# Kernel tuning notes

Measured on AMD Instinct MI355X. Metric: run time of the kernel, lower is better.

## Reference

```python
import jax, jax.numpy as jnp
import numpy as np

B, S, D, H, HD = 4, 2048, 1024, 16, 64


def setup_inputs() -> dict:
    key = jax.random.key(0)
    k1, k2, k3 = jax.random.split(key, 3)
    x = jax.random.normal(k1, (B, S, D), dtype=jnp.float32)
    w_attn = jax.random.normal(k2, (D, 3, H, HD), dtype=jnp.float32) * 0.02
    b_attn = jnp.zeros((3, H, HD), dtype=jnp.float32)
    w_proj = jax.random.normal(k3, (H, HD, D), dtype=jnp.float32) * 0.02
    b_proj = jnp.zeros((D,), dtype=jnp.float32)
    return {"x": x, "w_attn": w_attn, "b_attn": b_attn, "w_proj": w_proj, "b_proj": b_proj}


def reference(x, w_attn, b_attn, w_proj, b_proj):
    # c_attn: [B,S,D] x [D,3,H,HD] -> [B,3,H,S,HD]
    qkv = jnp.einsum('bsd,dqhe->bqhse', x, w_attn) + b_attn[None, :, :, None, :]
    q, k, v = qkv[:, 0], qkv[:, 1], qkv[:, 2]  # each [B,H,S,HD]
    scale = 1.0 / jnp.sqrt(jnp.asarray(HD, dtype=q.dtype))
    scores = jnp.einsum('bhse,bhte->bhst', q * scale, k)  # [B,H,S,S]
    causal = jnp.tril(jnp.ones((S, S), dtype=bool))
    scores = jnp.where(causal, scores, jnp.asarray(-1e9, dtype=scores.dtype))
    attn = jax.nn.softmax(scores, axis=-1)
    out = jnp.einsum('bhst,bhte->bhse', attn, v)  # [B,H,S,HD]
    # c_proj: contract (heads, head_size) -> embed
    return jnp.einsum('bhse,hed->bsd', out, w_proj) + b_proj
```

## Files before the change

kernel.cpp:

```cpp
#include <hip/hip_runtime.h>

#define NB 4
#define NS 2048
#define ND 1024
#define NH 16
#define NE 64
#define NM (NB*NS)

typedef __attribute__((ext_vector_type(8))) __bf16 bf16x8;
typedef __attribute__((ext_vector_type(4))) float f32x4;

__device__ __forceinline__ float bf2f(unsigned short h) {
  union { unsigned u; float f; } c; c.u = ((unsigned)h) << 16; return c.f;
}
__device__ __forceinline__ unsigned short f2bf(float f) {
  union { float f; unsigned u; } c; c.f = f;
  return (unsigned short)((c.u + 0x7fffu + ((c.u >> 16) & 1u)) >> 16);
}
__device__ __forceinline__ void load16_to_lds(const void* g, void* l) {
  __builtin_amdgcn_global_load_lds(
      (__attribute__((address_space(1))) void*)(void*)(unsigned long long)(const char*)g,
      (__attribute__((address_space(3))) void*)l, 16, 0, 0);
}

__global__ void detect_dtype(const unsigned* __restrict__ x, int* __restrict__ flag) {
  __shared__ int cnt;
  if (threadIdx.x == 0) cnt = 0;
  __syncthreads();
  unsigned w = x[((unsigned)threadIdx.x * 16381u) & ((1u << 21) - 1u)];
  unsigned lo = w & 0xFFFFu;
  int e = (int)((lo >> 7) & 0xFF);
  int plausible = (lo == 0u) || (e >= 100 && e <= 142);
  atomicAdd(&cnt, plausible);
  __syncthreads();
  if (threadIdx.x == 0) *flag = (cnt >= 192) ? 1 : 0;
}

__global__ void conv_to_bf16(const void* __restrict__ src, unsigned short* __restrict__ dst,
                             int n, const int* __restrict__ flag) {
  int stride = gridDim.x * blockDim.x;
  int i0 = blockIdx.x * blockDim.x + threadIdx.x;
  if (*flag) {
    const unsigned short* s = (const unsigned short*)src;
    for (int i = i0; i < n; i += stride) dst[i] = s[i];
  } else {
    const float* s = (const float*)src;
    for (int i = i0; i < n; i += stride) dst[i] = f2bf(s[i]);
  }
}

__global__ __launch_bounds__(256) void transpose_conv(const void* __restrict__ in,
                                                      unsigned short* __restrict__ out,
                                                      int K, int N, const int* __restrict__ flag) {
  __shared__ unsigned short tile[32][33];
  int n0 = blockIdx.x * 32, k0 = blockIdx.y * 32;
  int tx = threadIdx.x, ty = threadIdx.y;
  if (*flag) {
    const unsigned short* p = (const unsigned short*)in;
#pragma unroll
    for (int i = 0; i < 4; ++i)
      tile[ty + 8*i][tx] = p[(size_t)(k0 + ty + 8*i) * N + n0 + tx];
  } else {
    const float* p = (const float*)in;
#pragma unroll
    for (int i = 0; i < 4; ++i)
      tile[ty + 8*i][tx] = f2bf(p[(size_t)(k0 + ty + 8*i) * N + n0 + tx]);
  }
  __syncthreads();
#pragma unroll
  for (int i = 0; i < 4; ++i)
    out[(size_t)(n0 + ty + 8*i) * K + k0 + tx] = tile[tx][ty + 8*i];
}

#define BUFB 49152

__device__ __forceinline__ void gemm_core_v5(const unsigned short* __restrict__ Ag,
                                             const unsigned short* __restrict__ Btg,
                                             int m0, int n0,
                                             unsigned short* sm,
                                             f32x4 (&acc)[4][4]) {
  char* smb = (char*)sm;
  const int t = threadIdx.x;
  const int lane = t & 63, w = t >> 6;
  const int wr = w >> 1, wc = w & 1;
  const int frm = lane & 15, qd = lane >> 4;
  const int px0 = ((qd    ) ^ (frm & 7)) * 16;
  const int px1 = ((4 + qd) ^ (frm & 7)) * 16;
  const int NT = ND / 64;

  auto stage = [&](int kt, int b) {
    char* Ab = smb + b * BUFB;
    char* Bb = Ab + 32768;
    int kk = kt * 64;
#pragma unroll
    for (int u = 0; u < 4; ++u) {
      int ci = u * 512 + t;
      int row = ci >> 3, c = ci & 7, l = c ^ (row & 7);
      load16_to_lds(Ag + (size_t)(m0 + row) * ND + kk + l * 8, Ab + ci * 16);
    }
#pragma unroll
    for (int u = 0; u < 2; ++u) {
      int ci = u * 512 + t;
      int row = ci >> 3, c = ci & 7, l = c ^ (row & 7);
      load16_to_lds(Btg + (size_t)(n0 + row) * ND + kk + l * 8, Bb + ci * 16);
    }
  };

  stage(0, 0);
  asm volatile("s_waitcnt vmcnt(0)\n\ts_barrier" ::: "memory");

  for (int kt = 0; kt < NT; ++kt) {
    const int cur = kt & 1;
    const char* Ab = smb + cur * BUFB;
    const char* Bb = Ab + 32768;

    if (kt + 1 < NT) stage(kt + 1, cur ^ 1);

    bf16x8 a[4][2], b[4][2];
#pragma unroll
    for (int i = 0; i < 4; ++i) {
      int row = 64*wr + 16*i + frm;
      a[i][0] = *(const bf16x8*)(Ab + row * 128 + px0);
      a[i][1] = *(const bf16x8*)(Ab + row * 128 + px1);
    }
#pragma unroll
    for (int j = 0; j < 4; ++j) {
      int row = 64*wc + 16*j + frm;
      b[j][0] = *(const bf16x8*)(Bb + row * 128 + px0);
      b[j][1] = *(const bf16x8*)(Bb + row * 128 + px1);
    }
    asm volatile("s_waitcnt lgkmcnt(0)" ::: "memory");
    __builtin_amdgcn_s_setprio(1);
#pragma unroll
    for (int i = 0; i < 4; ++i)
#pragma unroll
      for (int j = 0; j < 4; ++j) {
        acc[i][j] = __builtin_amdgcn_mfma_f32_16x16x32_bf16(a[i][0], b[j][0], acc[i][j], 0, 0, 0);
        acc[i][j] = __builtin_amdgcn_mfma_f32_16x16x32_bf16(a[i][1], b[j][1], acc[i][j], 0, 0, 0);
      }
    __builtin_amdgcn_s_setprio(0);
    if (kt + 1 < NT)
      asm volatile("s_waitcnt vmcnt(0)\n\ts_barrier" ::: "memory");
  }
}

__global__ __launch_bounds__(512, 2) void gemm_qkv_v5(const unsigned short* __restrict__ X,
                                                      const unsigned short* __restrict__ W1T,
                                                      const unsigned short* __restrict__ battn,
                                                      unsigned short* __restrict__ qb,
                                                      unsigned short* __restrict__ kb,
                                                      unsigned short* __restrict__ vb) {
  __shared__ unsigned short sm[2 * 384 * 64];
  int flat = blockIdx.x + 24 * blockIdx.y;
  int virt = (flat & 7) * 96 + (flat >> 3);
  const int n0 = (virt % 24) * 128;
  const int m0 = (virt / 24) * 256;

  f32x4 acc[4][4] = {};
  gemm_core_v5(X, W1T, m0, n0, sm, acc);

  const int t = threadIdx.x, lane = t & 63, w = t >> 6;
  const int wr = w >> 1, wc = w & 1;
  const int coln = lane & 15, rbase = (lane >> 4) * 4;
#pragma unroll
  for (int j = 0; j < 4; ++j) {
    int nn = n0 + 64*wc + 16*j + coln;
    int qq = nn >> 10;
    int h  = (nn >> 6) & 15;
    int e  = nn & 63;
    float bias = bf2f(battn[nn]);
    float scale = (qq == 0) ? (0.125f * 1.44269504f) : 1.0f;
    if (qq == 2) {
#pragma unroll
      for (int i = 0; i < 4; ++i) {
        int mm0 = m0 + 64*wr + 16*i + rbase;
        int bb = mm0 >> 11, s0 = mm0 & 2047;
        unsigned long long pk = 0;
#pragma unroll
        for (int rr = 0; rr < 4; ++rr) {
          float v = acc[i][j][rr] + bias;
          pk |= ((unsigned long long)f2bf(v)) << (16 * rr);
        }
        size_t idx = (((size_t)bb * NH + h) * NE + e) * NS + s0;
        *(unsigned long long*)(vb + idx) = pk;
      }
    } else {
      unsigned short* dst = (qq == 0) ? qb : kb;
#pragma unroll
      for (int i = 0; i < 4; ++i) {
#pragma unroll
        for (int rr = 0; rr < 4; ++rr) {
          int mm = m0 + 64*wr + 16*i + rbase + rr;
          int bb = mm >> 11, s = mm & 2047;
          float v = (acc[i][j][rr] + bias) * scale;
          dst[(((size_t)bb * NH + h) * NS + s) * NE + e] = f2bf(v);
        }
      }
    }
  }
}

__global__ __launch_bounds__(512, 2) void gemm_proj_v5(const unsigned short* __restrict__ A,
                                                       const unsigned short* __restrict__ W2T,
                                                       const unsigned short* __restrict__ bproj,
                                                       void* __restrict__ outv,
                                                       const int* __restrict__ flag) {
  __shared__ unsigned short sm[2 * 384 * 64];
  int flat = blockIdx.x + 8 * blockIdx.y;
  int virt = (flat & 7) * 32 + (flat >> 3);
  const int n0 = (virt % 8) * 128;
  const int m0 = (virt / 8) * 256;

  f32x4 acc[4][4] = {};
  gemm_core_v5(A, W2T, m0, n0, sm, acc);

  const int isbf = *flag;
  unsigned short* out16 = (unsigned short*)outv;
  float* out32 = (float*)outv;
  const int t = threadIdx.x, lane = t & 63, w = t >> 6;
  const int wr = w >> 1, wc = w & 1;
  const int coln = lane & 15, rbase = (lane >> 4) * 4;
#pragma unroll
  for (int j = 0; j < 4; ++j) {
    int nn = n0 + 64*wc + 16*j + coln;
    float bias = bf2f(bproj[nn]);
#pragma unroll
    for (int i = 0; i < 4; ++i) {
#pragma unroll
      for (int rr = 0; rr < 4; ++rr) {
        int mm = m0 + 64*wr + 16*i + rbase + rr;
        float v = acc[i][j][rr] + bias;
        if (isbf) out16[(size_t)mm * ND + nn] = f2bf(v);
        else      out32[(size_t)mm * ND + nn] = v;
      }
    }
  }
}

__global__ __launch_bounds__(256, 4) void attn_causal(const unsigned short* __restrict__ qb,
                                                      const unsigned short* __restrict__ kb,
                                                      const unsigned short* __restrict__ vtb,
                                                      unsigned short* __restrict__ ob) {
  __shared__ unsigned short QPs[128 * 64];
  __shared__ unsigned short Ks[2][32 * 64];
  __shared__ unsigned short Vt[2][32 * 64];

  int t = threadIdx.x, lane = t & 63, w = t >> 6;
  int qd = lane >> 4, li = lane & 15;
  int sw0 = ((qd ^ (li & 7)) * 8);
  int sw1 = (((4 + qd) ^ (li & 7)) * 8);

  const int qtab[4][4] = {{15,8,7,0},{14,9,6,1},{13,10,5,2},{12,11,4,3}};
  int bi = blockIdx.x;
  int bh = bi & 63;
  int qt = qtab[(bi >> 6) & 3][bi >> 8];
  int q0 = qt * 128;
  int NT = 4 * qt + 4;
  size_t base = (size_t)bh * NS * NE;
  int bb = bh >> 4, hh = bh & 15;

  bf16x8 onesf;
#pragma unroll
  for (int j = 0; j < 8; ++j) onesf[j] = (__bf16)1.0f;

  auto stage_kv = [&](int kt, int buf) {
    int k0 = kt * 32;
    int r = t >> 3, p = t & 7, l = p ^ (r & 7);
    load16_to_lds(kb + base + (size_t)(k0 + r) * NE + l * 8, (char*)Ks[buf] + t * 16);
    int e = 2 * r + (l >> 2);
    load16_to_lds(vtb + base + (size_t)e * NS + k0 + (l & 3) * 8, (char*)Vt[buf] + t * 16);
  };

#pragma unroll
  for (int c = 0; c < 4; ++c) {
    int ch = c * 256 + t;
    int r = ch >> 3, jl = (ch & 7) ^ (r & 7);
    load16_to_lds(qb + base + (size_t)(q0 + r) * NE + jl * 8, (char*)QPs + ch * 16);
  }
  stage_kv(0, 0);
  asm volatile("s_waitcnt vmcnt(2)\n\ts_barrier" ::: "memory");

  bf16x8 qa[2][2];
#pragma unroll
  for (int i = 0; i < 2; ++i) {
    const unsigned short* qr = QPs + (32*w + 16*i + li) * 64;
    qa[i][0] = *(const bf16x8*)(qr + sw0);
    qa[i][1] = *(const bf16x8*)(qr + sw1);
  }

  f32x4 o[2][4] = {};
  float l_run[2][4] = {};

  for (int kt = 0; kt < NT; ++kt) {
    int cur = kt & 1;
    asm volatile("s_waitcnt lgkmcnt(0)\n\ts_barrier" ::: "memory");
    if (kt + 1 < NT) {
      stage_kv(kt + 1, cur ^ 1);
      asm volatile("s_waitcnt vmcnt(2)\n\ts_barrier" ::: "memory");
    } else {
      asm volatile("s_waitcnt vmcnt(0)\n\ts_barrier" ::: "memory");
    }

    int k0 = kt * 32;
    const unsigned short* Ksc = Ks[cur];
    const unsigned short* Vtc = Vt[cur];

    bf16x8 kfr[2][2];
#pragma unroll
    for (int c = 0; c < 2; ++c) {
      const unsigned short* kr = Ksc + (16*c + li) * 64;
      kfr[c][0] = *(const bf16x8*)(kr + sw0);
      kfr[c][1] = *(const bf16x8*)(kr + sw1);
    }

    int need_mask = (k0 >= q0);
#pragma unroll
    for (int i = 0; i < 2; ++i) {
#pragma unroll
      for (int c = 0; c < 2; ++c) {
        f32x4 s = {};
        s = __builtin_amdgcn_mfma_f32_16x16x32_bf16(qa[i][0], kfr[c][0], s, 0, 0, 0);
        s = __builtin_amdgcn_mfma_f32_16x16x32_bf16(qa[i][1], kfr[c][1], s, 0, 0, 0);
#pragma unroll
        for (int rr = 0; rr < 4; ++rr) {
          float pv = exp2f(s[rr]);
          if (need_mask) {
            int colk = k0 + 16*c + li;
            int rowq = q0 + 32*w + 16*i + qd*4 + rr;
            if (colk > rowq) pv = 0.f;
          }
          int prow = 32*w + 16*i + qd*4 + rr;
          int lo = 2*c + (li >> 3);
          QPs[prow * 64 + ((lo ^ (prow & 7)) * 8) + (li & 7)] =
              (unsigned short)(__float_as_uint(pv) >> 16);
        }
      }
    }

    bf16x8 pa[2];
#pragma unroll
    for (int i = 0; i < 2; ++i)
      pa[i] = *(const bf16x8*)(QPs + (32*w + 16*i + li) * 64 + sw0);

#pragma unroll
    for (int i = 0; i < 2; ++i) {
      f32x4 sm = {};
      sm = __builtin_amdgcn_mfma_f32_16x16x32_bf16(pa[i], onesf, sm, 0, 0, 0);
#pragma unroll
      for (int rr = 0; rr < 4; ++rr) l_run[i][rr] += sm[rr];
    }

#pragma unroll
    for (int c2 = 0; c2 < 4; ++c2) {
      const unsigned short* vr = Vtc + (8*c2 + (li >> 1)) * 64;
      bf16x8 vf = *(const bf16x8*)(vr + ((((li & 1) * 4 + qd) ^ ((li >> 1) & 7)) * 8));
#pragma unroll
      for (int i = 0; i < 2; ++i)
        o[i][c2] = __builtin_amdgcn_mfma_f32_16x16x32_bf16(pa[i], vf, o[i][c2], 0, 0, 0);
    }
  }

#pragma unroll
  for (int i = 0; i < 2; ++i)
#pragma unroll
    for (int c = 0; c < 4; ++c)
#pragma unroll
      for (int rr = 0; rr < 4; ++rr) {
        int rowm = 32*w + 16*i + qd*4 + rr;
        float inv = 1.0f / fmaxf(l_run[i][rr], 1e-30f);
        float ov = o[i][c][rr] * inv;
        int e = 16*c + li;
        ob[(((size_t)bb * NS + (q0 + rowm)) * NH + hh) * NE + e] = f2bf(ov);
      }
}

extern "C" void kernel_launch(void* const* d_in, const int* in_sizes, int n_in,
                              void* d_out, int out_size, void* d_ws, size_t ws_size,
                              hipStream_t stream) {
  (void)in_sizes; (void)n_in; (void)out_size; (void)ws_size;
  char* ws = (char*)d_ws;
  unsigned short* W1T = (unsigned short*)(ws);
  unsigned short* W2T = (unsigned short*)(ws + 6291456);
  unsigned short* qb  = (unsigned short*)(ws + 8388608);
  unsigned short* kb  = (unsigned short*)(ws + 25165824);
  unsigned short* vb  = (unsigned short*)(ws + 41943040);
  unsigned short* ob  = (unsigned short*)(ws + 58720256);
  unsigned short* bac = (unsigned short*)(ws + 75497472);
  unsigned short* bpc = (unsigned short*)(ws + 75505664);
  int*            flg = (int*)(ws + 75513856);
  unsigned short* xc  = ob;

  detect_dtype<<<1, 256, 0, stream>>>((const unsigned*)d_in[0], flg);
  conv_to_bf16<<<2048, 256, 0, stream>>>(d_in[0], xc,  NB*NS*ND, flg);
  conv_to_bf16<<<12,   256, 0, stream>>>(d_in[2], bac, 3*NH*NE, flg);
  conv_to_bf16<<<4,    256, 0, stream>>>(d_in[4], bpc, ND, flg);

  transpose_conv<<<dim3(3072/32, 1024/32), dim3(32, 8), 0, stream>>>(d_in[1], W1T, 1024, 3072, flg);
  transpose_conv<<<dim3(1024/32, 1024/32), dim3(32, 8), 0, stream>>>(d_in[3], W2T, 1024, 1024, flg);
  gemm_qkv_v5<<<dim3(3072/128, NM/256), 512, 0, stream>>>(xc, W1T, bac, qb, kb, vb);
  attn_causal<<<dim3(1024), 256, 0, stream>>>(qb, kb, vb, ob);
  gemm_proj_v5<<<dim3(1024/128, NM/256), 512, 0, stream>>>(ob, W2T, bpc, d_out, flg);
}
```

Baseline: 263.4 us.

## Enlarge attention tiles to 256 queries by 64 keys with 512-thread blocks

The causal attention kernel now has each block handle 256 query rows with 8 waves, and each step processes 64 keys instead of 32. Half as many blocks are launched, and the causal work-balancing table pairs short and long query chunks. Staging pointers are precomputed and advanced each step, the row-sum accumulation goes straight into an MFMA accumulator, and s_setprio raises wave priority around the MFMA sections. The aim is more K/V reuse per staged load and fewer barriers per key, at the cost of more LDS per block, fewer resident blocks, and coarser causal load balance.

```diff
diff --git a/kernel.cpp b/kernel.cpp
--- a/kernel.cpp
+++ b/kernel.cpp
@@ -237,25 +237,25 @@
   }
 }
 
-__global__ __launch_bounds__(256, 4) void attn_causal(const unsigned short* __restrict__ qb,
+__global__ __launch_bounds__(512, 4) void attn_causal(const unsigned short* __restrict__ qb,
                                                       const unsigned short* __restrict__ kb,
                                                       const unsigned short* __restrict__ vtb,
                                                       unsigned short* __restrict__ ob) {
-  __shared__ unsigned short QPs[128 * 64];
-  __shared__ unsigned short Ks[2][32 * 64];
-  __shared__ unsigned short Vt[2][32 * 64];
+  __shared__ unsigned short QPs[256 * 64];
+  __shared__ unsigned short Ks[2][64 * 64];
+  __shared__ unsigned short Vt[2][2 * 32 * 64];
 
   int t = threadIdx.x, lane = t & 63, w = t >> 6;
   int qd = lane >> 4, li = lane & 15;
   int sw0 = ((qd ^ (li & 7)) * 8);
   int sw1 = (((4 + qd) ^ (li & 7)) * 8);
 
-  const int qtab[4][4] = {{15,8,7,0},{14,9,6,1},{13,10,5,2},{12,11,4,3}};
+  const int tab[4][2] = {{0,7},{1,6},{2,5},{3,4}};
   int bi = blockIdx.x;
   int bh = bi & 63;
-  int qt = qtab[(bi >> 6) & 3][bi >> 8];
-  int q0 = qt * 128;
-  int NT = 4 * qt + 4;
+  int qc = tab[(bi >> 6) & 3][bi >> 8];
+  int q0 = qc * 256;
+  int NT = 4 * qc + 4;
   size_t base = (size_t)bh * NS * NE;
   int bb = bh >> 4, hh = bh & 15;
 
@@ -263,21 +263,31 @@
 #pragma unroll
   for (int j = 0; j < 8; ++j) onesf[j] = (__bf16)1.0f;
 
-  auto stage_kv = [&](int kt, int buf) {
-    int k0 = kt * 32;
-    int r = t >> 3, p = t & 7, l = p ^ (r & 7);
-    load16_to_lds(kb + base + (size_t)(k0 + r) * NE + l * 8, (char*)Ks[buf] + t * 16);
-    int e = 2 * r + (l >> 2);
-    load16_to_lds(vtb + base + (size_t)e * NS + k0 + (l & 3) * 8, (char*)Vt[buf] + t * 16);
+  int r8 = t >> 3;
+  int lswk = (t & 7) ^ (r8 & 7);
+  const char* ksrc = (const char*)(kb + base + (size_t)r8 * NE + lswk * 8);
+  char* kdst = (char*)Ks[0] + t * 16;
+  int sub = t >> 8, tt = t & 255;
+  int rv = tt >> 3;
+  int lswv = (tt & 7) ^ (rv & 7);
+  int ev = 2 * rv + (lswv >> 2);
+  const char* vsrc = (const char*)(vtb + base + (size_t)ev * NS + sub * 32 + (lswv & 3) * 8);
+  char* vdst = (char*)Vt[0] + sub * 4096 + tt * 16;
+
+  auto stage_kv = [&](int buf) {
+    load16_to_lds(ksrc, kdst + buf * 8192);
+    load16_to_lds(vsrc, vdst + buf * 8192);
+    ksrc += (size_t)64 * NE * 2;
+    vsrc += 64 * 2;
   };
 
 #pragma unroll
   for (int c = 0; c < 4; ++c) {
-    int ch = c * 256 + t;
+    int ch = c * 512 + t;
     int r = ch >> 3, jl = (ch & 7) ^ (r & 7);
     load16_to_lds(qb + base + (size_t)(q0 + r) * NE + jl * 8, (char*)QPs + ch * 16);
   }
-  stage_kv(0, 0);
+  stage_kv(0);
   asm volatile("s_waitcnt vmcnt(2)\n\ts_barrier" ::: "memory");
 
   bf16x8 qa[2][2];
@@ -289,35 +299,36 @@
   }
 
   f32x4 o[2][4] = {};
-  float l_run[2][4] = {};
+  f32x4 lacc[2] = {};
 
   for (int kt = 0; kt < NT; ++kt) {
     int cur = kt & 1;
     asm volatile("s_waitcnt lgkmcnt(0)\n\ts_barrier" ::: "memory");
     if (kt + 1 < NT) {
-      stage_kv(kt + 1, cur ^ 1);
+      stage_kv(cur ^ 1);
       asm volatile("s_waitcnt vmcnt(2)\n\ts_barrier" ::: "memory");
     } else {
       asm volatile("s_waitcnt vmcnt(0)\n\ts_barrier" ::: "memory");
     }
 
-    int k0 = kt * 32;
+    int k0 = kt * 64;
     const unsigned short* Ksc = Ks[cur];
     const unsigned short* Vtc = Vt[cur];
 
-    bf16x8 kfr[2][2];
-#pragma unroll
-    for (int c = 0; c < 2; ++c) {
+    bf16x8 kfr[4][2];
+#pragma unroll
+    for (int c = 0; c < 4; ++c) {
       const unsigned short* kr = Ksc + (16*c + li) * 64;
       kfr[c][0] = *(const bf16x8*)(kr + sw0);
       kfr[c][1] = *(const bf16x8*)(kr + sw1);
     }
 
-    int need_mask = (k0 >= q0);
+    int need_mask = (k0 + 63 > q0 + 32*w);
+    __builtin_amdgcn_s_setprio(1);
 #pragma unroll
     for (int i = 0; i < 2; ++i) {
 #pragma unroll
-      for (int c = 0; c < 2; ++c) {
+      for (int c = 0; c < 4; ++c) {
         f32x4 s = {};
         s = __builtin_amdgcn_mfma_f32_16x16x32_bf16(qa[i][0], kfr[c][0], s, 0, 0, 0);
         s = __builtin_amdgcn_mfma_f32_16x16x32_bf16(qa[i][1], kfr[c][1], s, 0, 0, 0);
@@ -331,33 +342,43 @@
           }
           int prow = 32*w + 16*i + qd*4 + rr;
           int lo = 2*c + (li >> 3);
-          QPs[prow * 64 + ((lo ^ (prow & 7)) * 8) + (li & 7)] =
+          *(unsigned short*)((char*)QPs +
+              (prow * 64 + ((lo ^ (prow & 7)) * 8) + (li & 7)) * 2) =
               (unsigned short)(__float_as_uint(pv) >> 16);
         }
       }
     }
-
-    bf16x8 pa[2];
-#pragma unroll
-    for (int i = 0; i < 2; ++i)
-      pa[i] = *(const bf16x8*)(QPs + (32*w + 16*i + li) * 64 + sw0);
-
+    __builtin_amdgcn_s_setprio(0);
+
+    bf16x8 pa[2][2];
 #pragma unroll
     for (int i = 0; i < 2; ++i) {
-      f32x4 sm = {};
-      sm = __builtin_amdgcn_mfma_f32_16x16x32_bf16(pa[i], onesf, sm, 0, 0, 0);
-#pragma unroll
-      for (int rr = 0; rr < 4; ++rr) l_run[i][rr] += sm[rr];
+      const unsigned short* pr = QPs + (32*w + 16*i + li) * 64;
+      pa[i][0] = *(const bf16x8*)(pr + sw0);
+      pa[i][1] = *(const bf16x8*)(pr + sw1);
+    }
+
+    __builtin_amdgcn_s_setprio(1);
+#pragma unroll
+    for (int i = 0; i < 2; ++i) {
+      lacc[i] = __builtin_amdgcn_mfma_f32_16x16x32_bf16(pa[i][0], onesf, lacc[i], 0, 0, 0);
+      lacc[i] = __builtin_amdgcn_mfma_f32_16x16x32_bf16(pa[i][1], onesf, lacc[i], 0, 0, 0);
     }
 
 #pragma unroll
     for (int c2 = 0; c2 < 4; ++c2) {
-      const unsigned short* vr = Vtc + (8*c2 + (li >> 1)) * 64;
-      bf16x8 vf = *(const bf16x8*)(vr + ((((li & 1) * 4 + qd) ^ ((li >> 1) & 7)) * 8));
-#pragma unroll
-      for (int i = 0; i < 2; ++i)
-        o[i][c2] = __builtin_amdgcn_mfma_f32_16x16x32_bf16(pa[i], vf, o[i][c2], 0, 0, 0);
-    }
+      const unsigned short* vr0 = Vtc + (8*c2 + (li >> 1)) * 64;
+      const unsigned short* vr1 = vr0 + 2048;
+      int vo = ((((li & 1) * 4 + qd) ^ ((li >> 1) & 7)) * 8);
+      bf16x8 vf0 = *(const bf16x8*)(vr0 + vo);
+      bf16x8 vf1 = *(const bf16x8*)(vr1 + vo);
+#pragma unroll
+      for (int i = 0; i < 2; ++i) {
+        o[i][c2] = __builtin_amdgcn_mfma_f32_16x16x32_bf16(pa[i][0], vf0, o[i][c2], 0, 0, 0);
+        o[i][c2] = __builtin_amdgcn_mfma_f32_16x16x32_bf16(pa[i][1], vf1, o[i][c2], 0, 0, 0);
+      }
+    }
+    __builtin_amdgcn_s_setprio(0);
   }
 
 #pragma unroll
@@ -367,7 +388,7 @@
 #pragma unroll
       for (int rr = 0; rr < 4; ++rr) {
         int rowm = 32*w + 16*i + qd*4 + rr;
-        float inv = 1.0f / fmaxf(l_run[i][rr], 1e-30f);
+        float inv = 1.0f / fmaxf(lacc[i][rr], 1e-30f);
         float ov = o[i][c][rr] * inv;
         int e = 16*c + li;
         ob[(((size_t)bb * NS + (q0 + rowm)) * NH + hh) * NE + e] = f2bf(ov);
@@ -398,6 +419,6 @@
   transpose_conv<<<dim3(3072/32, 1024/32), dim3(32, 8), 0, stream>>>(d_in[1], W1T, 1024, 3072, flg);
   transpose_conv<<<dim3(1024/32, 1024/32), dim3(32, 8), 0, stream>>>(d_in[3], W2T, 1024, 1024, flg);
   gemm_qkv_v5<<<dim3(3072/128, NM/256), 512, 0, stream>>>(xc, W1T, bac, qb, kb, vb);
-  attn_causal<<<dim3(1024), 256, 0, stream>>>(qb, kb, vb, ob);
+  attn_causal<<<dim3(512), 512, 0, stream>>>(qb, kb, vb, ob);
   gemm_proj_v5<<<dim3(1024/128, NM/256), 512, 0, stream>>>(ob, W2T, bpc, d_out, flg);
 }
```

After: 355.0 us. +34.8%, slower.

## Load Q/K/V fragments directly from global memory, dropping LDS staging and barriers

Applied to the files above, without the earlier changes.

The attention kernel no longer stages K and V tiles into double-buffered LDS with global_load_lds and barriers. Each wave now reads its MFMA fragments for Q, K and transposed V straight from global memory, and LDS holds only the P tile. The row-sum is also accumulated inside the MFMA accumulator instead of a separate float array. This removes the per-tile barriers and LDS traffic and cuts LDS use, which may allow more occupancy. The cost is that the four waves load the same K/V data redundantly and there is no explicit prefetch, so global load latency may be exposed.

```diff
diff --git a/kernel.cpp b/kernel.cpp
--- a/kernel.cpp
+++ b/kernel.cpp
@@ -241,14 +241,11 @@
                                                       const unsigned short* __restrict__ kb,
                                                       const unsigned short* __restrict__ vtb,
                                                       unsigned short* __restrict__ ob) {
-  __shared__ unsigned short QPs[128 * 64];
-  __shared__ unsigned short Ks[2][32 * 64];
-  __shared__ unsigned short Vt[2][32 * 64];
+  __shared__ unsigned short Ps[128 * 64];
 
   int t = threadIdx.x, lane = t & 63, w = t >> 6;
   int qd = lane >> 4, li = lane & 15;
   int sw0 = ((qd ^ (li & 7)) * 8);
-  int sw1 = (((4 + qd) ^ (li & 7)) * 8);
 
   const int qtab[4][4] = {{15,8,7,0},{14,9,6,1},{13,10,5,2},{12,11,4,3}};
   int bi = blockIdx.x;
@@ -259,58 +256,33 @@
   size_t base = (size_t)bh * NS * NE;
   int bb = bh >> 4, hh = bh & 15;
 
+  const unsigned short* kbase = kb + base;
+  const unsigned short* vbase = vtb + base;
+
   bf16x8 onesf;
 #pragma unroll
   for (int j = 0; j < 8; ++j) onesf[j] = (__bf16)1.0f;
 
-  auto stage_kv = [&](int kt, int buf) {
+  bf16x8 qa[2][2];
+#pragma unroll
+  for (int i = 0; i < 2; ++i) {
+    const unsigned short* qr = qb + base + (size_t)(q0 + 32*w + 16*i + li) * 64 + 8*qd;
+    qa[i][0] = *(const bf16x8*)(qr);
+    qa[i][1] = *(const bf16x8*)(qr + 32);
+  }
+
+  f32x4 o[2][4] = {};
+  f32x4 lacc[2] = {};
+
+  for (int kt = 0; kt < NT; ++kt) {
     int k0 = kt * 32;
-    int r = t >> 3, p = t & 7, l = p ^ (r & 7);
-    load16_to_lds(kb + base + (size_t)(k0 + r) * NE + l * 8, (char*)Ks[buf] + t * 16);
-    int e = 2 * r + (l >> 2);
-    load16_to_lds(vtb + base + (size_t)e * NS + k0 + (l & 3) * 8, (char*)Vt[buf] + t * 16);
-  };
-
-#pragma unroll
-  for (int c = 0; c < 4; ++c) {
-    int ch = c * 256 + t;
-    int r = ch >> 3, jl = (ch & 7) ^ (r & 7);
-    load16_to_lds(qb + base + (size_t)(q0 + r) * NE + jl * 8, (char*)QPs + ch * 16);
-  }
-  stage_kv(0, 0);
-  asm volatile("s_waitcnt vmcnt(2)\n\ts_barrier" ::: "memory");
-
-  bf16x8 qa[2][2];
-#pragma unroll
-  for (int i = 0; i < 2; ++i) {
-    const unsigned short* qr = QPs + (32*w + 16*i + li) * 64;
-    qa[i][0] = *(const bf16x8*)(qr + sw0);
-    qa[i][1] = *(const bf16x8*)(qr + sw1);
-  }
-
-  f32x4 o[2][4] = {};
-  float l_run[2][4] = {};
-
-  for (int kt = 0; kt < NT; ++kt) {
-    int cur = kt & 1;
-    asm volatile("s_waitcnt lgkmcnt(0)\n\ts_barrier" ::: "memory");
-    if (kt + 1 < NT) {
-      stage_kv(kt + 1, cur ^ 1);
-      asm volatile("s_waitcnt vmcnt(2)\n\ts_barrier" ::: "memory");
-    } else {
-      asm volatile("s_waitcnt vmcnt(0)\n\ts_barrier" ::: "memory");
-    }
-
-    int k0 = kt * 32;
-    const unsigned short* Ksc = Ks[cur];
-    const unsigned short* Vtc = Vt[cur];
 
     bf16x8 kfr[2][2];
 #pragma unroll
     for (int c = 0; c < 2; ++c) {
-      const unsigned short* kr = Ksc + (16*c + li) * 64;
-      kfr[c][0] = *(const bf16x8*)(kr + sw0);
-      kfr[c][1] = *(const bf16x8*)(kr + sw1);
+      const unsigned short* kr = kbase + (size_t)(k0 + 16*c + li) * 64 + 8*qd;
+      kfr[c][0] = *(const bf16x8*)(kr);
+      kfr[c][1] = *(const bf16x8*)(kr + 32);
     }
 
     int need_mask = (k0 >= q0);
@@ -331,7 +303,7 @@
           }
           int prow = 32*w + 16*i + qd*4 + rr;
           int lo = 2*c + (li >> 3);
-          QPs[prow * 64 + ((lo ^ (prow & 7)) * 8) + (li & 7)] =
+          Ps[prow * 64 + ((lo ^ (prow & 7)) * 8) + (li & 7)] =
               (unsigned short)(__float_as_uint(pv) >> 16);
         }
       }
@@ -340,20 +312,15 @@
     bf16x8 pa[2];
 #pragma unroll
     for (int i = 0; i < 2; ++i)
-      pa[i] = *(const bf16x8*)(QPs + (32*w + 16*i + li) * 64 + sw0);
-
-#pragma unroll
-    for (int i = 0; i < 2; ++i) {
-      f32x4 sm = {};
-      sm = __builtin_amdgcn_mfma_f32_16x16x32_bf16(pa[i], onesf, sm, 0, 0, 0);
-#pragma unroll
-      for (int rr = 0; rr < 4; ++rr) l_run[i][rr] += sm[rr];
-    }
+      pa[i] = *(const bf16x8*)(Ps + (32*w + 16*i + li) * 64 + sw0);
+
+#pragma unroll
+    for (int i = 0; i < 2; ++i)
+      lacc[i] = __builtin_amdgcn_mfma_f32_16x16x32_bf16(pa[i], onesf, lacc[i], 0, 0, 0);
 
 #pragma unroll
     for (int c2 = 0; c2 < 4; ++c2) {
-      const unsigned short* vr = Vtc + (8*c2 + (li >> 1)) * 64;
-      bf16x8 vf = *(const bf16x8*)(vr + ((((li & 1) * 4 + qd) ^ ((li >> 1) & 7)) * 8));
+      bf16x8 vf = *(const bf16x8*)(vbase + (size_t)(16*c2 + li) * NS + k0 + 8*qd);
 #pragma unroll
       for (int i = 0; i < 2; ++i)
         o[i][c2] = __builtin_amdgcn_mfma_f32_16x16x32_bf16(pa[i], vf, o[i][c2], 0, 0, 0);
@@ -367,7 +334,7 @@
 #pragma unroll
       for (int rr = 0; rr < 4; ++rr) {
         int rowm = 32*w + 16*i + qd*4 + rr;
-        float inv = 1.0f / fmaxf(l_run[i][rr], 1e-30f);
+        float inv = 1.0f / fmaxf(lacc[i][rr], 1e-30f);
         float ov = o[i][c][rr] * inv;
         int e = 16*c + li;
         ob[(((size_t)bb * NS + (q0 + rowm)) * NH + hh) * NE + e] = f2bf(ov);
```

Result: slower. 324.4 us (+23.1%).
